# Kernel tuning notes

Hardware: AMD Instinct MI355X
Metric: run time of the kernel (lower is better)

## Reference

```python
import jax, jax.numpy as jnp
import numpy as np
import math

B, T, EMB, HD = 4, 2048, 2048, 128
HALF = HD // 2


def setup_inputs() -> dict:
    key = jax.random.key(0)
    ks = jax.random.split(key, 4)
    x = jax.random.normal(ks[0], (B, T, EMB), dtype=jnp.float32)
    s = 1.0 / math.sqrt(EMB)
    Wq = jax.random.normal(ks[1], (EMB, HD), dtype=jnp.float32) * s
    Wk = jax.random.normal(ks[2], (EMB, HD), dtype=jnp.float32) * s
    Wv = jax.random.normal(ks[3], (EMB, HD), dtype=jnp.float32) * s
    # Standard RoPE rotation table: theta_i = 10000^(-2i/HD), angle = pos * theta
    inv_freq = 1.0 / (10000.0 ** (np.arange(0, HALF, dtype=np.float32) / HALF))
    angles = np.arange(T, dtype=np.float32)[:, None] * inv_freq[None, :]  # [T, HALF]
    rot_cos = jnp.asarray(np.cos(angles), dtype=jnp.float32)
    rot_sin = jnp.asarray(np.sin(angles), dtype=jnp.float32)
    # Additive causal mask: 0 on/below diagonal, -1e9 above
    NEG = -1e9
    mask = jnp.where(jnp.tril(jnp.ones((T, T), dtype=bool)), 0.0, NEG).astype(jnp.float32)
    return {"x": x, "Wq": Wq, "Wk": Wk, "Wv": Wv,
            "rot_cos": rot_cos, "rot_sin": rot_sin, "mask": mask}


def _apply_rope(q, rot_cos, rot_sin):
    # q: [B, T, HD]; view last dim as HALF complex pairs and rotate
    qp = q.reshape(q.shape[0], q.shape[1], HALF, 2)
    re, im = qp[..., 0], qp[..., 1]
    out_re = re * rot_cos - im * rot_sin  # broadcast [T,HALF] over batch
    out_im = re * rot_sin + im * rot_cos
    return jnp.stack([out_re, out_im], axis=-1).reshape(q.shape)


def reference(x, Wq, Wk, Wv, rot_cos, rot_sin, mask):
    Q = x @ Wq  # [B, T, HD]
    K = x @ Wk
    V = x @ Wv
    Q = _apply_rope(Q, rot_cos, rot_sin)
    K = _apply_rope(K, rot_cos, rot_sin)
    scores = jnp.einsum('bqd,bkd->bqk', Q, K) / math.sqrt(HD)
    probs = jax.nn.softmax(scores + mask, axis=-1)  # dropout is identity in eval
    return jnp.einsum('bqk,bkd->bqd', probs, V)
```

## Files before the change

### kernel.cpp

```cpp
#include <hip/hip_runtime.h>
#include <cstddef>
#include <cstdint>

#define T_SEQ 2048
#define EMB_D 2048
#define HD_D  128

typedef __attribute__((ext_vector_type(8))) short short8;
typedef __attribute__((ext_vector_type(4))) float f32x4;
typedef __attribute__((ext_vector_type(4))) unsigned short ushort4v;
typedef __attribute__((ext_vector_type(8))) unsigned short ushort8v;
typedef __attribute__((ext_vector_type(2))) unsigned int uint2v;

union frag_u { short8 s8; unsigned u[4]; };

static __device__ __forceinline__ unsigned short f2bf_rne(float f) {
    union { float f; unsigned u; } v; v.f = f;
    unsigned r = v.u + 0x7fffu + ((v.u >> 16) & 1u);
    return (unsigned short)(r >> 16);
}
static __device__ __forceinline__ unsigned short f2bf_fast(float f) {
    union { float f; unsigned u; } v; v.f = f;
    return (unsigned short)((v.u + 0x8000u) >> 16);
}
static __device__ __forceinline__ unsigned pk2(float a, float b) {
    union { float f; unsigned u; } x, y; x.f = a; y.f = b;
    return __builtin_amdgcn_perm(y.u + 0x8000u, x.u + 0x8000u, 0x07060302);
}
#define EXP2F(x) __builtin_amdgcn_exp2f(x)

__global__ __launch_bounds__(256) void prep_weights(
    const float* __restrict__ Wq, const float* __restrict__ Wk,
    const float* __restrict__ Wv, unsigned short* __restrict__ Wt)
{
    __shared__ __attribute__((aligned(16))) unsigned short tw[64 * 132];
    const int w = blockIdx.y;
    const int k0 = blockIdx.x * 64;
    const float* W = (w == 0) ? Wq : (w == 1) ? Wk : Wv;
    const int tid = threadIdx.x;
#pragma unroll
    for (int p = 0; p < 8; p++) {
        const int f = p * 256 + tid;
        const int row = f >> 5, c4 = f & 31;
        const float4 v = *(const float4*)&W[(size_t)(k0 + row) * HD_D + c4 * 4];
        ushort4v h = { f2bf_rne(v.x), f2bf_rne(v.y), f2bf_rne(v.z), f2bf_rne(v.w) };
        *(ushort4v*)&tw[row * 132 + c4 * 4] = h;
    }
    __syncthreads();
    const int n = tid >> 1, h = tid & 1;
    unsigned short* dst = Wt + (size_t)w * (HD_D * EMB_D) + (size_t)n * EMB_D + k0 + h * 32;
#pragma unroll
    for (int j = 0; j < 4; j++) {
        ushort8v o;
#pragma unroll
        for (int jj = 0; jj < 8; jj++) o[jj] = tw[(h * 32 + j * 8 + jj) * 132 + n];
        *(ushort8v*)&dst[j * 8] = o;
    }
}

__global__ __launch_bounds__(256, 1) void qkv_fused(
    const float* __restrict__ x, const unsigned short* __restrict__ Wt,
    const float* __restrict__ rcos, const float* __restrict__ rsin,
    unsigned short* __restrict__ Qb, unsigned short* __restrict__ Kb,
    unsigned short* __restrict__ Vt)
{
    __shared__ __attribute__((aligned(16))) unsigned short xa[2][32 * 72];
    const int m0 = blockIdx.x * 32;
    const int tid = threadIdx.x;
    const int lane = tid & 63, wave = tid >> 6;
    const int l15 = lane & 15, lq = lane >> 4;
    const int kf = lq * 8;

    const unsigned short* Bp[6];
#pragma unroll
    for (int j = 0; j < 6; j++) {
        const int col0 = wave * 96 + j * 16;
        const int wsel = col0 >> 7;
        Bp[j] = Wt + (size_t)wsel * (HD_D * EMB_D)
                   + (size_t)((col0 & 127) + l15) * EMB_D + kf;
    }

    const int sr  = tid >> 4;
    const int sc4 = (tid & 15) * 4;
    const float* xp = x + (size_t)m0 * EMB_D;

    f32x4 acc[2][6];
#pragma unroll
    for (int i = 0; i < 2; i++)
#pragma unroll
        for (int j = 0; j < 6; j++) acc[i][j] = (f32x4){0.f, 0.f, 0.f, 0.f};

    frag_u Bc[6][2], Bn[6][2];
#pragma unroll
    for (int j = 0; j < 6; j++)
#pragma unroll
        for (int ks = 0; ks < 2; ks++)
            Bc[j][ks].s8 = *(const short8*)(Bp[j] + ks * 32);
#pragma unroll
    for (int p = 0; p < 2; p++) {
        const float4 v = *(const float4*)&xp[(size_t)(sr + p * 16) * EMB_D + sc4];
        uint2v h = { pk2(v.x, v.y), pk2(v.z, v.w) };
        *(uint2v*)&xa[0][(sr + p * 16) * 72 + sc4] = h;
    }
    __syncthreads();

    for (int k0 = 0; k0 < EMB_D; k0 += 64) {
        const int buf = (k0 >> 6) & 1;
        const bool more = (k0 + 64) < EMB_D;
        float4 xn[2];
        if (more) {
#pragma unroll
            for (int p = 0; p < 2; p++)
                xn[p] = *(const float4*)&xp[(size_t)(sr + p * 16) * EMB_D + k0 + 64 + sc4];
#pragma unroll
            for (int j = 0; j < 6; j++)
#pragma unroll
                for (int ks = 0; ks < 2; ks++)
                    Bn[j][ks].s8 = *(const short8*)(Bp[j] + k0 + 64 + ks * 32);
        }
        frag_u A[2][2];
#pragma unroll
        for (int i = 0; i < 2; i++)
#pragma unroll
            for (int ks = 0; ks < 2; ks++)
                A[i][ks].s8 = *(const short8*)&xa[buf][(i * 16 + l15) * 72 + ks * 32 + kf];
#pragma unroll
        for (int ks = 0; ks < 2; ks++)
#pragma unroll
            for (int i = 0; i < 2; i++)
#pragma unroll
                for (int j = 0; j < 6; j++)
                    acc[i][j] = __builtin_amdgcn_mfma_f32_16x16x32_bf16(
                        A[i][ks].s8, Bc[j][ks].s8, acc[i][j], 0, 0, 0);
        if (more) {
#pragma unroll
            for (int p = 0; p < 2; p++) {
                uint2v h = { pk2(xn[p].x, xn[p].y), pk2(xn[p].z, xn[p].w) };
                *(uint2v*)&xa[buf ^ 1][(sr + p * 16) * 72 + sc4] = h;
            }
#pragma unroll
            for (int j = 0; j < 6; j++)
#pragma unroll
                for (int ks = 0; ks < 2; ks++)
                    Bc[j][ks] = Bn[j][ks];
            __syncthreads();
        }
    }

    const float qscale = 0.08838834764831845f * 1.4426950408889634f;
#pragma unroll
    for (int i = 0; i < 2; i++) {
#pragma unroll
        for (int r = 0; r < 4; r++) {
            const int row = m0 + i * 16 + lq * 4 + r;
            const int t = row & (T_SEQ - 1);
            const int bb = row >> 11;
#pragma unroll
            for (int j = 0; j < 6; j++) {
                const int col = wave * 96 + j * 16 + l15;
                const int mat = col >> 7, mcol = col & 127;
                const float v = acc[i][j][r];
                if (mat == 2) {
                    Vt[((size_t)bb * HD_D + mcol) * T_SEQ + t] = f2bf_rne(v);
                } else {
                    const int ip = mcol >> 1;
                    const float c = rcos[t * 64 + ip];
                    const float s = rsin[t * 64 + ip];
                    const float pv = __shfl_xor(v, 1);
                    float rv = (mcol & 1) ? (pv * s + v * c) : (v * c - pv * s);
                    if (mat == 0) {
                        rv *= qscale;
                        Qb[(size_t)row * HD_D + mcol] = f2bf_rne(rv);
                    } else {
                        Kb[(size_t)row * HD_D + mcol] = f2bf_rne(rv);
                    }
                }
            }
        }
    }
}

__global__ __launch_bounds__(256, 2) void attn(
    const unsigned short* __restrict__ Qb, const unsigned short* __restrict__ Kb,
    const unsigned short* __restrict__ Vt, float* __restrict__ out)
{
    __shared__ float O_s[4][16 * 128];
    __shared__ __attribute__((aligned(16))) unsigned short P_s[4][16 * 40];
    __shared__ float l_s[4][16];

    const int tid = threadIdx.x;
    const int lane = tid & 63, wave = tid >> 6;
    const int l15 = lane & 15, lq = lane >> 4;
    const int kf = lq * 8;

    const int b  = blockIdx.x & 3;
    const int q0 = (127 - (blockIdx.x >> 2)) * 16;
    const int kend = q0 + 16;
    const float M2 = 16.0f;

    const unsigned short* Qp = Qb + (size_t)(b * T_SEQ + q0) * HD_D;
    short8 aQ[4];
#pragma unroll
    for (int d = 0; d < 4; d++)
        aQ[d] = *(const short8*)&Qp[l15 * HD_D + d * 32 + kf];

    f32x4 acc[8];
#pragma unroll
    for (int d = 0; d < 8; d++) acc[d] = (f32x4){0.f, 0.f, 0.f, 0.f};
    float l_r[4] = {0.f, 0.f, 0.f, 0.f};

    const unsigned short* Kbase = Kb + (size_t)b * T_SEQ * HD_D;
    const unsigned short* Vbase = Vt + (size_t)b * HD_D * T_SEQ;
    unsigned short* Pw = &P_s[wave][0];

    int c = wave;
    bool have = (c * 32) < kend;
    short8 Kn[8];
    if (have) {
        const unsigned short* Kp = Kbase + (size_t)(c * 32) * HD_D;
#pragma unroll
        for (int d = 0; d < 4; d++)
#pragma unroll
            for (int n = 0; n < 2; n++)
                Kn[d * 2 + n] = *(const short8*)&Kp[(size_t)(n * 16 + l15) * HD_D + d * 32 + kf];
    }

    while (have) {
        const int k0 = c * 32;
        short8 Kc[8];
#pragma unroll
        for (int i = 0; i < 8; i++) Kc[i] = Kn[i];
        const int cn = c + 4;
        const bool hn = (cn * 32) < kend;

        f32x4 s0 = (f32x4){0.f, 0.f, 0.f, 0.f};
        f32x4 s1 = (f32x4){0.f, 0.f, 0.f, 0.f};
#pragma unroll
        for (int d = 0; d < 4; d++) {
            s0 = __builtin_amdgcn_mfma_f32_16x16x32_bf16(aQ[d], Kc[d * 2 + 0], s0, 0, 0, 0);
            s1 = __builtin_amdgcn_mfma_f32_16x16x32_bf16(aQ[d], Kc[d * 2 + 1], s1, 0, 0, 0);
        }

        if (hn) {
            const unsigned short* Kp = Kbase + (size_t)(cn * 32) * HD_D;
#pragma unroll
            for (int d = 0; d < 4; d++)
#pragma unroll
                for (int n = 0; n < 2; n++)
                    Kn[d * 2 + n] = *(const short8*)&Kp[(size_t)(n * 16 + l15) * HD_D + d * 32 + kf];
        }
        short8 Vc[8];
#pragma unroll
        for (int d = 0; d < 8; d++)
            Vc[d] = *(const short8*)&Vbase[(size_t)(d * 16 + l15) * T_SEQ + k0 + kf];

#pragma unroll
        for (int r = 0; r < 4; r++) {
            const int q = q0 + lq * 4 + r;
            const float p0 = ((k0 + l15)      <= q) ? EXP2F(s0[r] - M2) : 0.f;
            const float p1 = ((k0 + 16 + l15) <= q) ? EXP2F(s1[r] - M2) : 0.f;
            l_r[r] += p0 + p1;
            const int prow = (lq * 4 + r) * 40;
            Pw[prow + l15]      = f2bf_fast(p0);
            Pw[prow + 16 + l15] = f2bf_fast(p1);
        }
        const short8 pA = *(const short8*)&Pw[l15 * 40 + kf];
#pragma unroll
        for (int d = 0; d < 8; d++)
            acc[d] = __builtin_amdgcn_mfma_f32_16x16x32_bf16(pA, Vc[d], acc[d], 0, 0, 0);

        c = cn; have = hn;
    }

#pragma unroll
    for (int r = 0; r < 4; r++) {
        float lr = l_r[r];
        lr += __shfl_xor(lr, 1);
        lr += __shfl_xor(lr, 2);
        lr += __shfl_xor(lr, 4);
        lr += __shfl_xor(lr, 8);
        if (l15 == 0) l_s[wave][lq * 4 + r] = lr;
#pragma unroll
        for (int d = 0; d < 8; d++)
            O_s[wave][(lq * 4 + r) * 128 + d * 16 + l15] = acc[d][r];
    }
    __syncthreads();

    const int row = tid >> 4;
    const int dc = (tid & 15) * 8;
    const float lt = l_s[0][row] + l_s[1][row] + l_s[2][row] + l_s[3][row];
    const float inv = 1.0f / lt;
    f32x4 o0 = (f32x4){0.f, 0.f, 0.f, 0.f};
    f32x4 o1 = (f32x4){0.f, 0.f, 0.f, 0.f};
#pragma unroll
    for (int w2 = 0; w2 < 4; w2++) {
        const float* p = &O_s[w2][row * 128 + dc];
        o0 += *(const f32x4*)p;
        o1 += *(const f32x4*)(p + 4);
    }
    float* op = out + (size_t)(b * T_SEQ + q0 + row) * HD_D + dc;
    *(f32x4*)op       = o0 * inv;
    *(f32x4*)(op + 4) = o1 * inv;
}

extern "C" void kernel_launch(void* const* d_in, const int* in_sizes, int n_in,
                              void* d_out, int out_size, void* d_ws, size_t ws_size,
                              hipStream_t stream)
{
    (void)in_sizes; (void)n_in; (void)out_size; (void)ws_size;
    const float* x  = (const float*)d_in[0];
    const float* Wq = (const float*)d_in[1];
    const float* Wk = (const float*)d_in[2];
    const float* Wv = (const float*)d_in[3];
    const float* rc = (const float*)d_in[4];
    const float* rs = (const float*)d_in[5];
    float* out = (float*)d_out;

    char* ws = (char*)d_ws;
    unsigned short* Wt = (unsigned short*)(ws);
    unsigned short* Qb = (unsigned short*)(ws + 1572864);
    unsigned short* Kb = (unsigned short*)(ws + 1572864 + 2097152);
    unsigned short* Vt = (unsigned short*)(ws + 1572864 + 2 * 2097152);

    prep_weights<<<dim3(32, 3), 256, 0, stream>>>(Wq, Wk, Wv, Wt);
    qkv_fused   <<<dim3(256),   256, 0, stream>>>(x, Wt, rc, rs, Qb, Kb, Vt);
    attn        <<<dim3(512),   256, 0, stream>>>(Qb, Kb, Vt, out);
}
```

Baseline: 213.3 us.

## Stage QKV GEMM tiles via direct global-to-LDS loads and unroll attention loop by two

The QKV projection kernel drops its register-prefetched double buffer. It now loads x (fp32) and the bf16 weight tile straight into swizzled shared memory with global_load_lds, converting x to bf16 when building fragments. The attention kernel processes two K/V chunks per loop iteration, with separate P staging buffers, so more loads and MFMAs are in flight. The trade-off is that the GEMM loop loses its explicit prefetch overlap and now syncs twice per step, while the weight tile adds 48KB of LDS per block. The attention loop uses more registers.

```diff
diff --git a/kernel.cpp b/kernel.cpp
--- a/kernel.cpp
+++ b/kernel.cpp
@@ -10,7 +10,6 @@
 typedef __attribute__((ext_vector_type(4))) float f32x4;
 typedef __attribute__((ext_vector_type(4))) unsigned short ushort4v;
 typedef __attribute__((ext_vector_type(8))) unsigned short ushort8v;
-typedef __attribute__((ext_vector_type(2))) unsigned int uint2v;
 
 union frag_u { short8 s8; unsigned u[4]; };
 
@@ -26,6 +25,11 @@
 static __device__ __forceinline__ unsigned pk2(float a, float b) {
     union { float f; unsigned u; } x, y; x.f = a; y.f = b;
     return __builtin_amdgcn_perm(y.u + 0x8000u, x.u + 0x8000u, 0x07060302);
+}
+static __device__ __forceinline__ void dma16(const void* g, void* l) {
+    __builtin_amdgcn_global_load_lds(
+        (const __attribute__((address_space(1))) unsigned int*)g,
+        (__attribute__((address_space(3))) unsigned int*)l, 16, 0, 0);
 }
 #define EXP2F(x) __builtin_amdgcn_exp2f(x)
 
@@ -64,25 +68,49 @@
     unsigned short* __restrict__ Qb, unsigned short* __restrict__ Kb,
     unsigned short* __restrict__ Vt)
 {
-    __shared__ __attribute__((aligned(16))) unsigned short xa[2][32 * 72];
+    __shared__ __attribute__((aligned(16))) float xs[32 * 64];
+    __shared__ __attribute__((aligned(16))) unsigned short wsb[384 * 64];
     const int m0 = blockIdx.x * 32;
     const int tid = threadIdx.x;
     const int lane = tid & 63, wave = tid >> 6;
     const int l15 = lane & 15, lq = lane >> 4;
-    const int kf = lq * 8;
-
-    const unsigned short* Bp[6];
-#pragma unroll
-    for (int j = 0; j < 6; j++) {
-        const int col0 = wave * 96 + j * 16;
-        const int wsel = col0 >> 7;
-        Bp[j] = Wt + (size_t)wsel * (HD_D * EMB_D)
-                   + (size_t)((col0 & 127) + l15) * EMB_D + kf;
-    }
-
-    const int sr  = tid >> 4;
-    const int sc4 = (tid & 15) * 4;
-    const float* xp = x + (size_t)m0 * EMB_D;
+
+    const float* xSrc[2]; float* xDst[2];
+#pragma unroll
+    for (int p = 0; p < 2; p++) {
+        const int g = p * 256 + tid;
+        const int row = g >> 4, c = g & 15;
+        xSrc[p] = x + (size_t)(m0 + row) * EMB_D + (c ^ (row & 15)) * 4;
+        xDst[p] = xs + (size_t)(p * 256 + wave * 64) * 4;
+    }
+    const unsigned short* wSrc[12]; unsigned short* wDst[12];
+#pragma unroll
+    for (int p = 0; p < 12; p++) {
+        const int g = p * 256 + tid;
+        const int n = g >> 3, c = g & 7;
+        wSrc[p] = Wt + (size_t)n * EMB_D + (c ^ (n & 7)) * 8;
+        wDst[p] = wsb + (size_t)(p * 256 + wave * 64) * 8;
+    }
+
+    int offA[2][2][2];
+#pragma unroll
+    for (int i = 0; i < 2; i++)
+#pragma unroll
+        for (int ks = 0; ks < 2; ks++) {
+            const int row = i * 16 + l15;
+            const int ga = ks * 8 + lq * 2;
+            offA[i][ks][0] = row * 64 + ((ga)     ^ (row & 15)) * 4;
+            offA[i][ks][1] = row * 64 + ((ga + 1) ^ (row & 15)) * 4;
+        }
+    int offB[6][2];
+#pragma unroll
+    for (int j = 0; j < 6; j++)
+#pragma unroll
+        for (int ks = 0; ks < 2; ks++) {
+            const int n = wave * 96 + j * 16 + l15;
+            const int gb = ks * 4 + lq;
+            offB[j][ks] = n * 64 + (gb ^ (n & 7)) * 8;
+        }
 
     f32x4 acc[2][6];
 #pragma unroll
@@ -90,61 +118,36 @@
 #pragma unroll
         for (int j = 0; j < 6; j++) acc[i][j] = (f32x4){0.f, 0.f, 0.f, 0.f};
 
-    frag_u Bc[6][2], Bn[6][2];
-#pragma unroll
-    for (int j = 0; j < 6; j++)
+    for (int k0 = 0; k0 < EMB_D; k0 += 64) {
+        __syncthreads();
+#pragma unroll
+        for (int p = 0; p < 2; p++)  dma16(xSrc[p] + k0, xDst[p]);
+#pragma unroll
+        for (int p = 0; p < 12; p++) dma16(wSrc[p] + k0, wDst[p]);
+        __syncthreads();
+
+        frag_u A[2][2];
+#pragma unroll
+        for (int i = 0; i < 2; i++)
+#pragma unroll
+            for (int ks = 0; ks < 2; ks++) {
+                const f32x4 f0 = *(const f32x4*)&xs[offA[i][ks][0]];
+                const f32x4 f1 = *(const f32x4*)&xs[offA[i][ks][1]];
+                A[i][ks].u[0] = pk2(f0.x, f0.y);
+                A[i][ks].u[1] = pk2(f0.z, f0.w);
+                A[i][ks].u[2] = pk2(f1.x, f1.y);
+                A[i][ks].u[3] = pk2(f1.z, f1.w);
+            }
 #pragma unroll
         for (int ks = 0; ks < 2; ks++)
-            Bc[j][ks].s8 = *(const short8*)(Bp[j] + ks * 32);
-#pragma unroll
-    for (int p = 0; p < 2; p++) {
-        const float4 v = *(const float4*)&xp[(size_t)(sr + p * 16) * EMB_D + sc4];
-        uint2v h = { pk2(v.x, v.y), pk2(v.z, v.w) };
-        *(uint2v*)&xa[0][(sr + p * 16) * 72 + sc4] = h;
-    }
-    __syncthreads();
-
-    for (int k0 = 0; k0 < EMB_D; k0 += 64) {
-        const int buf = (k0 >> 6) & 1;
-        const bool more = (k0 + 64) < EMB_D;
-        float4 xn[2];
-        if (more) {
-#pragma unroll
-            for (int p = 0; p < 2; p++)
-                xn[p] = *(const float4*)&xp[(size_t)(sr + p * 16) * EMB_D + k0 + 64 + sc4];
-#pragma unroll
-            for (int j = 0; j < 6; j++)
-#pragma unroll
-                for (int ks = 0; ks < 2; ks++)
-                    Bn[j][ks].s8 = *(const short8*)(Bp[j] + k0 + 64 + ks * 32);
-        }
-        frag_u A[2][2];
-#pragma unroll
-        for (int i = 0; i < 2; i++)
-#pragma unroll
-            for (int ks = 0; ks < 2; ks++)
-                A[i][ks].s8 = *(const short8*)&xa[buf][(i * 16 + l15) * 72 + ks * 32 + kf];
-#pragma unroll
-        for (int ks = 0; ks < 2; ks++)
-#pragma unroll
-            for (int i = 0; i < 2; i++)
-#pragma unroll
-                for (int j = 0; j < 6; j++)
+#pragma unroll
+            for (int j = 0; j < 6; j++) {
+                const short8 B = *(const short8*)&wsb[offB[j][ks]];
+#pragma unroll
+                for (int i = 0; i < 2; i++)
                     acc[i][j] = __builtin_amdgcn_mfma_f32_16x16x32_bf16(
-                        A[i][ks].s8, Bc[j][ks].s8, acc[i][j], 0, 0, 0);
-        if (more) {
-#pragma unroll
-            for (int p = 0; p < 2; p++) {
-                uint2v h = { pk2(xn[p].x, xn[p].y), pk2(xn[p].z, xn[p].w) };
-                *(uint2v*)&xa[buf ^ 1][(sr + p * 16) * 72 + sc4] = h;
-            }
-#pragma unroll
-            for (int j = 0; j < 6; j++)
-#pragma unroll
-                for (int ks = 0; ks < 2; ks++)
-                    Bc[j][ks] = Bn[j][ks];
-            __syncthreads();
-        }
+                        A[i][ks].s8, B, acc[i][j], 0, 0, 0);
+            }
     }
 
     const float qscale = 0.08838834764831845f * 1.4426950408889634f;
@@ -185,7 +188,7 @@
     const unsigned short* __restrict__ Vt, float* __restrict__ out)
 {
     __shared__ float O_s[4][16 * 128];
-    __shared__ __attribute__((aligned(16))) unsigned short P_s[4][16 * 40];
+    __shared__ __attribute__((aligned(16))) unsigned short P_s[4][2][16 * 40];
     __shared__ float l_s[4][16];
 
     const int tid = threadIdx.x;
@@ -211,65 +214,84 @@
 
     const unsigned short* Kbase = Kb + (size_t)b * T_SEQ * HD_D;
     const unsigned short* Vbase = Vt + (size_t)b * HD_D * T_SEQ;
-    unsigned short* Pw = &P_s[wave][0];
-
-    int c = wave;
-    bool have = (c * 32) < kend;
-    short8 Kn[8];
-    if (have) {
-        const unsigned short* Kp = Kbase + (size_t)(c * 32) * HD_D;
+    unsigned short* PwA = &P_s[wave][0][0];
+    unsigned short* PwB = &P_s[wave][1][0];
+
+    for (int c = wave; c * 32 < kend; c += 8) {
+        const int kA = c * 32;
+        const int kB = (c + 4) * 32;
+        const bool hB = kB < kend;
+
+        const unsigned short* KpA = Kbase + (size_t)kA * HD_D;
+        const unsigned short* KpB = Kbase + (size_t)kB * HD_D;
+        short8 KA[8], KB_[8];
 #pragma unroll
         for (int d = 0; d < 4; d++)
 #pragma unroll
             for (int n = 0; n < 2; n++)
-                Kn[d * 2 + n] = *(const short8*)&Kp[(size_t)(n * 16 + l15) * HD_D + d * 32 + kf];
-    }
-
-    while (have) {
-        const int k0 = c * 32;
-        short8 Kc[8];
-#pragma unroll
-        for (int i = 0; i < 8; i++) Kc[i] = Kn[i];
-        const int cn = c + 4;
-        const bool hn = (cn * 32) < kend;
-
-        f32x4 s0 = (f32x4){0.f, 0.f, 0.f, 0.f};
-        f32x4 s1 = (f32x4){0.f, 0.f, 0.f, 0.f};
+                KA[d * 2 + n] = *(const short8*)&KpA[(size_t)(n * 16 + l15) * HD_D + d * 32 + kf];
+        if (hB) {
+#pragma unroll
+            for (int d = 0; d < 4; d++)
+#pragma unroll
+                for (int n = 0; n < 2; n++)
+                    KB_[d * 2 + n] = *(const short8*)&KpB[(size_t)(n * 16 + l15) * HD_D + d * 32 + kf];
+        }
+
+        f32x4 sA0 = (f32x4){0.f, 0.f, 0.f, 0.f}, sA1 = sA0, sB0 = sA0, sB1 = sA0;
 #pragma unroll
         for (int d = 0; d < 4; d++) {
-            s0 = __builtin_amdgcn_mfma_f32_16x16x32_bf16(aQ[d], Kc[d * 2 + 0], s0, 0, 0, 0);
-            s1 = __builtin_amdgcn_mfma_f32_16x16x32_bf16(aQ[d], Kc[d * 2 + 1], s1, 0, 0, 0);
-        }
-
-        if (hn) {
-            const unsigned short* Kp = Kbase + (size_t)(cn * 32) * HD_D;
-#pragma unroll
-            for (int d = 0; d < 4; d++)
-#pragma unroll
-                for (int n = 0; n < 2; n++)
-                    Kn[d * 2 + n] = *(const short8*)&Kp[(size_t)(n * 16 + l15) * HD_D + d * 32 + kf];
-        }
-        short8 Vc[8];
+            sA0 = __builtin_amdgcn_mfma_f32_16x16x32_bf16(aQ[d], KA[d * 2 + 0], sA0, 0, 0, 0);
+            sA1 = __builtin_amdgcn_mfma_f32_16x16x32_bf16(aQ[d], KA[d * 2 + 1], sA1, 0, 0, 0);
+        }
+        if (hB) {
+#pragma unroll
+            for (int d = 0; d < 4; d++) {
+                sB0 = __builtin_amdgcn_mfma_f32_16x16x32_bf16(aQ[d], KB_[d * 2 + 0], sB0, 0, 0, 0);
+                sB1 = __builtin_amdgcn_mfma_f32_16x16x32_bf16(aQ[d], KB_[d * 2 + 1], sB1, 0, 0, 0);
+            }
+        }
+
+        short8 VA[8];
 #pragma unroll
         for (int d = 0; d < 8; d++)
-            Vc[d] = *(const short8*)&Vbase[(size_t)(d * 16 + l15) * T_SEQ + k0 + kf];
+            VA[d] = *(const short8*)&Vbase[(size_t)(d * 16 + l15) * T_SEQ + kA + kf];
 
 #pragma unroll
         for (int r = 0; r < 4; r++) {
             const int q = q0 + lq * 4 + r;
-            const float p0 = ((k0 + l15)      <= q) ? EXP2F(s0[r] - M2) : 0.f;
-            const float p1 = ((k0 + 16 + l15) <= q) ? EXP2F(s1[r] - M2) : 0.f;
+            const float p0 = ((kA + l15)      <= q) ? EXP2F(sA0[r] - M2) : 0.f;
+            const float p1 = ((kA + 16 + l15) <= q) ? EXP2F(sA1[r] - M2) : 0.f;
             l_r[r] += p0 + p1;
             const int prow = (lq * 4 + r) * 40;
-            Pw[prow + l15]      = f2bf_fast(p0);
-            Pw[prow + 16 + l15] = f2bf_fast(p1);
-        }
-        const short8 pA = *(const short8*)&Pw[l15 * 40 + kf];
+            PwA[prow + l15]      = f2bf_fast(p0);
+            PwA[prow + 16 + l15] = f2bf_fast(p1);
+        }
+        const short8 pA = *(const short8*)&PwA[l15 * 40 + kf];
 #pragma unroll
         for (int d = 0; d < 8; d++)
-            acc[d] = __builtin_amdgcn_mfma_f32_16x16x32_bf16(pA, Vc[d], acc[d], 0, 0, 0);
-
-        c = cn; have = hn;
+            acc[d] = __builtin_amdgcn_mfma_f32_16x16x32_bf16(pA, VA[d], acc[d], 0, 0, 0);
+
+        if (hB) {
+            short8 VB[8];
+#pragma unroll
+            for (int d = 0; d < 8; d++)
+                VB[d] = *(const short8*)&Vbase[(size_t)(d * 16 + l15) * T_SEQ + kB + kf];
+#pragma unroll
+            for (int r = 0; r < 4; r++) {
+                const int q = q0 + lq * 4 + r;
+                const float p0 = ((kB + l15)      <= q) ? EXP2F(sB0[r] - M2) : 0.f;
+                const float p1 = ((kB + 16 + l15) <= q) ? EXP2F(sB1[r] - M2) : 0.f;
+                l_r[r] += p0 + p1;
+                const int prow = (lq * 4 + r) * 40;
+                PwB[prow + l15]      = f2bf_fast(p0);
+                PwB[prow + 16 + l15] = f2bf_fast(p1);
+            }
+            const short8 pB = *(const short8*)&PwB[l15 * 40 + kf];
+#pragma unroll
+            for (int d = 0; d < 8; d++)
+                acc[d] = __builtin_amdgcn_mfma_f32_16x16x32_bf16(pB, VB[d], acc[d], 0, 0, 0);
+        }
     }
 
 #pragma unroll
```

New measurement: 203.5 us. 1.05x faster.
